# Kernel tuning notes

Measured on AMD Instinct MI355X. Metric: run time of the kernel, lower is better.

Reference implementation:

```python
import jax, jax.numpy as jnp
import numpy as np

N_NODES = 100000
N_EDGES = 1600000
D_IN = 128
D_OUT = 128


def setup_inputs() -> dict:
    key = jax.random.key(0)
    k1, k2, k3, k4, k5, k6 = jax.random.split(key, 6)
    x = jax.random.normal(k1, (N_NODES, D_IN), dtype=jnp.float32)
    adj_rows = jnp.sort(jax.random.randint(k2, (N_EDGES,), 0, N_NODES, dtype=jnp.int32))
    adj_cols = jax.random.randint(k3, (N_EDGES,), 0, N_NODES, dtype=jnp.int32)
    adj_vals = jax.random.uniform(k4, (N_EDGES,), dtype=jnp.float32)
    weight = jax.random.normal(k5, (D_OUT, D_IN), dtype=jnp.float32) * (1.0 / np.sqrt(D_IN))
    bias = jax.random.normal(k6, (D_OUT,), dtype=jnp.float32) * 0.01
    return {"x": x, "adj_rows": adj_rows, "adj_cols": adj_cols,
            "adj_vals": adj_vals, "weight": weight, "bias": bias}


def reference(x, adj_rows, adj_cols, adj_vals, weight, bias):
    # w_input = inputs @ W.T  -> [N, D_OUT]
    w_input = x @ weight.T
    # SpMM: out[r] = sum_e adj_vals[e] * w_input[cols[e]] for edges with rows[e] == r
    msgs = adj_vals[:, None] * w_input[adj_cols]          # [E, D_OUT]
    agg = jax.ops.segment_sum(msgs, adj_rows, num_segments=N_NODES)
    out = jax.nn.relu(agg + bias)
    return out.astype(jnp.float32)
```

## Files before the change

kernel.cpp:

```cpp
#include <hip/hip_runtime.h>
#include <hip/hip_bf16.h>

#define D 128
#define RPW 8

typedef __attribute__((ext_vector_type(8))) short bf16x8;
typedef __attribute__((ext_vector_type(4))) float f32x4;

__device__ __forceinline__ unsigned short f2bf(float f) {
    union { float f; unsigned u; } uf{f};
    unsigned r = uf.u + 0x7fffu + ((uf.u >> 16) & 1u);
    return (unsigned short)(r >> 16);
}
__device__ __forceinline__ unsigned packcv(float a, float b) {
    __hip_bfloat162 h = __float22bfloat162_rn(make_float2(a, b));
    union { __hip_bfloat162 h; unsigned u; } c{h};
    return c.u;
}
__device__ __forceinline__ float bflo(unsigned u) {
    union { unsigned u; float f; } c{u << 16};
    return c.f;
}
__device__ __forceinline__ float bfhi(unsigned u) {
    union { unsigned u; float f; } c{u & 0xffff0000u};
    return c.f;
}

#define FMA8(A, vv, u) \
    A[0] = fmaf(vv, bflo(u.x), A[0]); A[1] = fmaf(vv, bfhi(u.x), A[1]); \
    A[2] = fmaf(vv, bflo(u.y), A[2]); A[3] = fmaf(vv, bfhi(u.y), A[3]); \
    A[4] = fmaf(vv, bflo(u.z), A[4]); A[5] = fmaf(vv, bfhi(u.z), A[5]); \
    A[6] = fmaf(vv, bflo(u.w), A[6]); A[7] = fmaf(vv, bfhi(u.w), A[7]);

__global__ __launch_bounds__(256) void build_rowptr(const int* __restrict__ rows,
                                                    const float* __restrict__ W,
                                                    unsigned short* __restrict__ wbf,
                                                    int2* __restrict__ rowptr,
                                                    int e, int n) {
    int i = blockIdx.x * 256 + threadIdx.x;
    if (i < D * D) wbf[i] = f2bf(W[i]);
    if (i >= e) return;
    int r = rows[i];
    int prev = (i == 0) ? -1 : rows[i - 1];
    int next = (i == e - 1) ? n : rows[i + 1];
    if (prev != r) {
        rowptr[r].x = i;
        for (int q = prev + 1; q < r; ++q) rowptr[q] = make_int2(i, i);
    }
    if (next != r) {
        rowptr[r].y = i + 1;
        if (i == e - 1)
            for (int q = r + 1; q < n; ++q) rowptr[q] = make_int2(e, e);
    }
}

__global__ __launch_bounds__(256) void gemm_mfma(const float* __restrict__ x,
                                                 const unsigned short* __restrict__ wbf,
                                                 unsigned short* __restrict__ wi,
                                                 int nrows) {
    __shared__ __align__(16) unsigned short Ws[128 * 128];

    const int tid = threadIdx.x;
#pragma unroll
    for (int it = 0; it < 8; ++it) {
        int elem = it * 2048 + tid * 8;
        int r = elem >> 7, k = elem & 127;
        int idx = (r * 128 + k) ^ ((r & 7) << 3);
        *(uint4*)&Ws[idx] = *(const uint4*)(wbf + elem);
    }
    __syncthreads();

    const int lane = tid & 63;
    const int row0 = blockIdx.x * 128 + (tid >> 6) * 32;
    const int lrow = lane & 15;
    const int lk8 = (lane >> 4) * 8;

    bf16x8 xfrag[2][4];
#pragma unroll
    for (int xb = 0; xb < 2; ++xb)
#pragma unroll
        for (int kb = 0; kb < 4; ++kb) {
            int gr = min(row0 + xb * 16 + lrow, nrows - 1);
            const float4* p = (const float4*)(x + (size_t)gr * D + kb * 32 + lk8);
            float4 f0 = p[0], f1 = p[1];
            union { bf16x8 v; unsigned u[4]; } cv;
            cv.u[0] = packcv(f0.x, f0.y);
            cv.u[1] = packcv(f0.z, f0.w);
            cv.u[2] = packcv(f1.x, f1.y);
            cv.u[3] = packcv(f1.z, f1.w);
            xfrag[xb][kb] = cv.v;
        }

    f32x4 acc[2][8];
#pragma unroll
    for (int xb = 0; xb < 2; ++xb)
#pragma unroll
        for (int cb = 0; cb < 8; ++cb)
            acc[xb][cb] = (f32x4){0.f, 0.f, 0.f, 0.f};

#pragma unroll
    for (int cb = 0; cb < 8; ++cb) {
#pragma unroll
        for (int kb = 0; kb < 4; ++kb) {
            int wrow = cb * 16 + lrow;
            int idx = (wrow * 128 + kb * 32 + lk8) ^ ((wrow & 7) << 3);
            bf16x8 wfrag = *(const bf16x8*)&Ws[idx];
            acc[0][cb] = __builtin_amdgcn_mfma_f32_16x16x32_bf16(wfrag, xfrag[0][kb], acc[0][cb], 0, 0, 0);
            acc[1][cb] = __builtin_amdgcn_mfma_f32_16x16x32_bf16(wfrag, xfrag[1][kb], acc[1][cb], 0, 0, 0);
        }
    }

#pragma unroll
    for (int xb = 0; xb < 2; ++xb) {
        int g = row0 + xb * 16 + lrow;
        if (g < nrows) {
#pragma unroll
            for (int cb = 0; cb < 8; ++cb) {
                uint2 o;
                o.x = packcv(acc[xb][cb][0], acc[xb][cb][1]);
                o.y = packcv(acc[xb][cb][2], acc[xb][cb][3]);
                *(uint2*)(wi + (size_t)g * D + cb * 16 + (lane >> 4) * 4) = o;
            }
        }
    }
}

__global__ __launch_bounds__(256) void spmm_relu(const unsigned short* __restrict__ wi,
                                                 const int2* __restrict__ rowptr,
                                                 const int* __restrict__ cols,
                                                 const float* __restrict__ vals,
                                                 const float* __restrict__ bias,
                                                 float* __restrict__ out,
                                                 int n) {
    const int lane = threadIdx.x & 63;
    const int R0 = (blockIdx.x * 4 + (threadIdx.x >> 6)) * RPW;
    if (R0 >= n) return;
    const int nr = min(RPW, n - R0);

    const int2 rp = rowptr[R0 + min(lane, nr - 1)];
    const int ch = (lane & 15) * 8;
    const int sub = lane >> 4;

    float4 b0 = *(const float4*)(bias + (lane & 15) * 8);
    float4 b1 = *(const float4*)(bias + (lane & 15) * 8 + 4);

    int st = __shfl(rp.x, 0), en = __shfl(rp.y, 0);
    int c = 0; float v = 0.f;
    { int idx = st + lane; if (idx < en) { c = cols[idx]; v = vals[idx]; } }

    for (int j = 0; j < nr; ++j) {
        int st_n = 0, en_n = 0, c_n = 0; float v_n = 0.f;
        if (j + 1 < nr) {
            st_n = __shfl(rp.x, j + 1); en_n = __shfl(rp.y, j + 1);
            int idx = st_n + lane; if (idx < en_n) { c_n = cols[idx]; v_n = vals[idx]; }
        }

        float a0[8] = {0.f, 0.f, 0.f, 0.f, 0.f, 0.f, 0.f, 0.f};
        float a1[8] = {0.f, 0.f, 0.f, 0.f, 0.f, 0.f, 0.f, 0.f};

        const int cnt = min(en - st, 64);
        if (cnt > 0) {
            int cA[4], cB[4];
            float vA[4], vB[4];
#pragma unroll
            for (int p = 0; p < 4; ++p) {
                cA[p] = __shfl(c, sub + 4 * p);       vA[p] = __shfl(v, sub + 4 * p);
                cB[p] = __shfl(c, 16 + sub + 4 * p);  vB[p] = __shfl(v, 16 + sub + 4 * p);
            }
            uint4 uA[4], uB[4];
#pragma unroll
            for (int p = 0; p < 4; ++p) uA[p] = *(const uint4*)(wi + (size_t)cA[p] * D + ch);
#pragma unroll
            for (int p = 0; p < 4; ++p) uB[p] = *(const uint4*)(wi + (size_t)cB[p] * D + ch);
#pragma unroll
            for (int p = 0; p < 4; ++p) {
                FMA8(a0, vA[p], uA[p]);
                FMA8(a1, vB[p], uB[p]);
            }
            for (int E = 32; E < cnt; E += 16) {
#pragma unroll
                for (int p = 0; p < 4; ++p) {
                    int   cq = __shfl(c, E + sub + 4 * p);
                    float vq = __shfl(v, E + sub + 4 * p);
                    uint4 uq = *(const uint4*)(wi + (size_t)cq * D + ch);
                    FMA8(a0, vq, uq);
                }
            }
        }
        for (int base = st + 64; base < en; base += 64) {
            int cc = 0; float vv = 0.f;
            { int idx = base + lane; if (idx < en) { cc = cols[idx]; vv = vals[idx]; } }
            const int cnt2 = min(en - base, 64);
            for (int E = 0; E < cnt2; E += 16) {
#pragma unroll
                for (int p = 0; p < 4; ++p) {
                    int   cq = __shfl(cc, E + sub + 4 * p);
                    float vq = __shfl(vv, E + sub + 4 * p);
                    uint4 uq = *(const uint4*)(wi + (size_t)cq * D + ch);
                    FMA8(a1, vq, uq);
                }
            }
        }

        float r8[8];
#pragma unroll
        for (int t = 0; t < 8; ++t) {
            float s = a0[t] + a1[t];
            s += __shfl_xor(s, 16);
            s += __shfl_xor(s, 32);
            r8[t] = s;
        }
        if (lane < 16) {
            float4 o0, o1;
            o0.x = fmaxf(r8[0] + b0.x, 0.f);
            o0.y = fmaxf(r8[1] + b0.y, 0.f);
            o0.z = fmaxf(r8[2] + b0.z, 0.f);
            o0.w = fmaxf(r8[3] + b0.w, 0.f);
            o1.x = fmaxf(r8[4] + b1.x, 0.f);
            o1.y = fmaxf(r8[5] + b1.y, 0.f);
            o1.z = fmaxf(r8[6] + b1.z, 0.f);
            o1.w = fmaxf(r8[7] + b1.w, 0.f);
            *(float4*)(out + (size_t)(R0 + j) * D + lane * 8) = o0;
            *(float4*)(out + (size_t)(R0 + j) * D + lane * 8 + 4) = o1;
        }

        st = st_n; en = en_n; c = c_n; v = v_n;
    }
}

extern "C" void kernel_launch(void* const* d_in, const int* in_sizes, int n_in,
                              void* d_out, int out_size, void* d_ws, size_t ws_size,
                              hipStream_t stream) {
    const float* x        = (const float*)d_in[0];
    const int*   adj_rows = (const int*)d_in[1];
    const int*   adj_cols = (const int*)d_in[2];
    const float* adj_vals = (const float*)d_in[3];
    const float* weight   = (const float*)d_in[4];
    const float* bias     = (const float*)d_in[5];
    float*       out      = (float*)d_out;

    const int n = in_sizes[0] / D;
    const int e = in_sizes[1];

    unsigned short* wi = (unsigned short*)d_ws;
    size_t off = ((size_t)n * D * sizeof(unsigned short) + 255) & ~(size_t)255;
    int2* rowptr = (int2*)((char*)d_ws + off);
    unsigned short* wbf = (unsigned short*)(rowptr + n);

    build_rowptr<<<(e + 255) / 256, 256, 0, stream>>>(adj_rows, weight, wbf,
                                                      rowptr, e, n);

    gemm_mfma<<<(n + 127) / 128, 256, 0, stream>>>(x, wbf, wi, n);

    spmm_relu<<<(n + 4 * RPW - 1) / (4 * RPW), 256, 0, stream>>>(
        wi, rowptr, adj_cols, adj_vals, bias, out, n);
}
```

Baseline: 96.14 us.

## Pack edge cols and bf16 vals into one word; shrink rows per wave; prefetch x before W staging

The rowptr kernel now packs each edge's column index (17 bits) and a bf16-rounded value into a single 32-bit word. The SpMM reads this one array instead of separate cols and vals, which halves the per-edge index traffic and the shuffle count. Rows per wave drop from 8 to 2 so more waves run in parallel, and the GEMM issues its x loads before staging W into LDS to overlap the two. Edge weights now carry bf16 precision, and column indices are limited to below 2^17.

New measurement: 94.31 us. No clear change (-1.9%).

```diff
diff --git a/kernel.cpp b/kernel.cpp
--- a/kernel.cpp
+++ b/kernel.cpp
@@ -2,7 +2,7 @@
 #include <hip/hip_bf16.h>
 
 #define D 128
-#define RPW 8
+#define RPW 2
 
 typedef __attribute__((ext_vector_type(8))) short bf16x8;
 typedef __attribute__((ext_vector_type(4))) float f32x4;
@@ -23,6 +23,11 @@
 }
 __device__ __forceinline__ float bfhi(unsigned u) {
     union { unsigned u; float f; } c{u & 0xffff0000u};
+    return c.f;
+}
+__device__ __forceinline__ int pc_col(unsigned u) { return (int)(u & 0x1FFFFu); }
+__device__ __forceinline__ float pc_val(unsigned u) {
+    union { unsigned u; float f; } c{(u >> 1) & 0xFFFF0000u};
     return c.f;
 }
 
@@ -33,13 +38,19 @@
     A[6] = fmaf(vv, bflo(u.w), A[6]); A[7] = fmaf(vv, bfhi(u.w), A[7]);
 
 __global__ __launch_bounds__(256) void build_rowptr(const int* __restrict__ rows,
+                                                    const int* __restrict__ cols,
+                                                    const float* __restrict__ vals,
                                                     const float* __restrict__ W,
                                                     unsigned short* __restrict__ wbf,
+                                                    unsigned* __restrict__ pc,
                                                     int2* __restrict__ rowptr,
                                                     int e, int n) {
     int i = blockIdx.x * 256 + threadIdx.x;
     if (i < D * D) wbf[i] = f2bf(W[i]);
     if (i >= e) return;
+
+    pc[i] = ((unsigned)f2bf(vals[i]) << 17) | (unsigned)cols[i];
+
     int r = rows[i];
     int prev = (i == 0) ? -1 : rows[i - 1];
     int next = (i == e - 1) ? n : rows[i + 1];
@@ -61,6 +72,22 @@
     __shared__ __align__(16) unsigned short Ws[128 * 128];
 
     const int tid = threadIdx.x;
+    const int lane = tid & 63;
+    const int row0 = blockIdx.x * 128 + (tid >> 6) * 32;
+    const int lrow = lane & 15;
+    const int lk8 = (lane >> 4) * 8;
+
+    float4 xf[2][4][2];
+#pragma unroll
+    for (int xb = 0; xb < 2; ++xb)
+#pragma unroll
+        for (int kb = 0; kb < 4; ++kb) {
+            int gr = min(row0 + xb * 16 + lrow, nrows - 1);
+            const float4* p = (const float4*)(x + (size_t)gr * D + kb * 32 + lk8);
+            xf[xb][kb][0] = p[0];
+            xf[xb][kb][1] = p[1];
+        }
+
 #pragma unroll
     for (int it = 0; it < 8; ++it) {
         int elem = it * 2048 + tid * 8;
@@ -70,19 +97,12 @@
     }
     __syncthreads();
 
-    const int lane = tid & 63;
-    const int row0 = blockIdx.x * 128 + (tid >> 6) * 32;
-    const int lrow = lane & 15;
-    const int lk8 = (lane >> 4) * 8;
-
     bf16x8 xfrag[2][4];
 #pragma unroll
     for (int xb = 0; xb < 2; ++xb)
 #pragma unroll
         for (int kb = 0; kb < 4; ++kb) {
-            int gr = min(row0 + xb * 16 + lrow, nrows - 1);
-            const float4* p = (const float4*)(x + (size_t)gr * D + kb * 32 + lk8);
-            float4 f0 = p[0], f1 = p[1];
+            float4 f0 = xf[xb][kb][0], f1 = xf[xb][kb][1];
             union { bf16x8 v; unsigned u[4]; } cv;
             cv.u[0] = packcv(f0.x, f0.y);
             cv.u[1] = packcv(f0.z, f0.w);
@@ -127,8 +147,7 @@
 
 __global__ __launch_bounds__(256) void spmm_relu(const unsigned short* __restrict__ wi,
                                                  const int2* __restrict__ rowptr,
-                                                 const int* __restrict__ cols,
-                                                 const float* __restrict__ vals,
+                                                 const unsigned* __restrict__ pc,
                                                  const float* __restrict__ bias,
                                                  float* __restrict__ out,
                                                  int n) {
@@ -145,14 +164,14 @@
     float4 b1 = *(const float4*)(bias + (lane & 15) * 8 + 4);
 
     int st = __shfl(rp.x, 0), en = __shfl(rp.y, 0);
-    int c = 0; float v = 0.f;
-    { int idx = st + lane; if (idx < en) { c = cols[idx]; v = vals[idx]; } }
+    unsigned u = 0;
+    { int idx = st + lane; if (idx < en) u = pc[idx]; }
 
     for (int j = 0; j < nr; ++j) {
-        int st_n = 0, en_n = 0, c_n = 0; float v_n = 0.f;
+        int st_n = 0, en_n = 0; unsigned u_n = 0;
         if (j + 1 < nr) {
             st_n = __shfl(rp.x, j + 1); en_n = __shfl(rp.y, j + 1);
-            int idx = st_n + lane; if (idx < en_n) { c_n = cols[idx]; v_n = vals[idx]; }
+            int idx = st_n + lane; if (idx < en_n) u_n = pc[idx];
         }
 
         float a0[8] = {0.f, 0.f, 0.f, 0.f, 0.f, 0.f, 0.f, 0.f};
@@ -160,44 +179,41 @@
 
         const int cnt = min(en - st, 64);
         if (cnt > 0) {
-            int cA[4], cB[4];
-            float vA[4], vB[4];
+            unsigned mA[4], mB[4];
 #pragma unroll
             for (int p = 0; p < 4; ++p) {
-                cA[p] = __shfl(c, sub + 4 * p);       vA[p] = __shfl(v, sub + 4 * p);
-                cB[p] = __shfl(c, 16 + sub + 4 * p);  vB[p] = __shfl(v, 16 + sub + 4 * p);
+                mA[p] = __shfl(u, sub + 4 * p);
+                mB[p] = __shfl(u, 16 + sub + 4 * p);
             }
             uint4 uA[4], uB[4];
 #pragma unroll
-            for (int p = 0; p < 4; ++p) uA[p] = *(const uint4*)(wi + (size_t)cA[p] * D + ch);
-#pragma unroll
-            for (int p = 0; p < 4; ++p) uB[p] = *(const uint4*)(wi + (size_t)cB[p] * D + ch);
+            for (int p = 0; p < 4; ++p) uA[p] = *(const uint4*)(wi + (size_t)pc_col(mA[p]) * D + ch);
+#pragma unroll
+            for (int p = 0; p < 4; ++p) uB[p] = *(const uint4*)(wi + (size_t)pc_col(mB[p]) * D + ch);
 #pragma unroll
             for (int p = 0; p < 4; ++p) {
-                FMA8(a0, vA[p], uA[p]);
-                FMA8(a1, vB[p], uB[p]);
+                FMA8(a0, pc_val(mA[p]), uA[p]);
+                FMA8(a1, pc_val(mB[p]), uB[p]);
             }
             for (int E = 32; E < cnt; E += 16) {
 #pragma unroll
                 for (int p = 0; p < 4; ++p) {
-                    int   cq = __shfl(c, E + sub + 4 * p);
-                    float vq = __shfl(v, E + sub + 4 * p);
-                    uint4 uq = *(const uint4*)(wi + (size_t)cq * D + ch);
-                    FMA8(a0, vq, uq);
+                    unsigned m = __shfl(u, E + sub + 4 * p);
+                    uint4 uq = *(const uint4*)(wi + (size_t)pc_col(m) * D + ch);
+                    FMA8(a0, pc_val(m), uq);
                 }
             }
         }
         for (int base = st + 64; base < en; base += 64) {
-            int cc = 0; float vv = 0.f;
-            { int idx = base + lane; if (idx < en) { cc = cols[idx]; vv = vals[idx]; } }
+            unsigned uu = 0;
+            { int idx = base + lane; if (idx < en) uu = pc[idx]; }
             const int cnt2 = min(en - base, 64);
             for (int E = 0; E < cnt2; E += 16) {
 #pragma unroll
                 for (int p = 0; p < 4; ++p) {
-                    int   cq = __shfl(cc, E + sub + 4 * p);
-                    float vq = __shfl(vv, E + sub + 4 * p);
-                    uint4 uq = *(const uint4*)(wi + (size_t)cq * D + ch);
-                    FMA8(a1, vq, uq);
+                    unsigned m = __shfl(uu, E + sub + 4 * p);
+                    uint4 uq = *(const uint4*)(wi + (size_t)pc_col(m) * D + ch);
+                    FMA8(a1, pc_val(m), uq);
                 }
             }
         }
@@ -224,7 +240,7 @@
             *(float4*)(out + (size_t)(R0 + j) * D + lane * 8 + 4) = o1;
         }
 
-        st = st_n; en = en_n; c = c_n; v = v_n;
+        st = st_n; en = en_n; u = u_n;
     }
 }
 
@@ -245,13 +261,14 @@
     unsigned short* wi = (unsigned short*)d_ws;
     size_t off = ((size_t)n * D * sizeof(unsigned short) + 255) & ~(size_t)255;
     int2* rowptr = (int2*)((char*)d_ws + off);
-    unsigned short* wbf = (unsigned short*)(rowptr + n);
-
-    build_rowptr<<<(e + 255) / 256, 256, 0, stream>>>(adj_rows, weight, wbf,
-                                                      rowptr, e, n);
+    unsigned* pc = (unsigned*)(rowptr + n);
+    unsigned short* wbf = (unsigned short*)(pc + e);
+
+    build_rowptr<<<(e + 255) / 256, 256, 0, stream>>>(adj_rows, adj_cols, adj_vals,
+                                                      weight, wbf, pc, rowptr, e, n);
 
     gemm_mfma<<<(n + 127) / 128, 256, 0, stream>>>(x, wbf, wi, n);
 
     spmm_relu<<<(n + 4 * RPW - 1) / (4 * RPW), 256, 0, stream>>>(
-        wi, rowptr, adj_cols, adj_vals, bias, out, n);
-}
+        wi, rowptr, pc, bias, out, n);
+}
```
